# Optimization experiments

Measured on AMD Instinct MI355X. Metric: run time of the kernel, lower is better.

The kernel has to match this reference:

```python
import jax, jax.numpy as jnp
import numpy as np

N = 50000      # nodes
E = 800000     # edges (avg degree 16)
IN = 128       # input feature dim
HID = 32       # per-head hidden dim
H = 4          # attention heads
C = 40         # num classes
SLOPE = 0.2    # leaky relu negative slope


def setup_inputs() -> dict:
    key = jax.random.key(0)
    ks = jax.random.split(key, 14)
    s = 0.05
    inputs = jax.random.normal(ks[0], (N, IN), jnp.float32)
    target = jax.random.normal(ks[1], (N, IN), jnp.float32)
    lamb = jax.random.uniform(ks[2], (1,), jnp.float32)
    src = jax.random.randint(ks[3], (E,), 0, N, jnp.int32)
    dst = jax.random.randint(ks[4], (E,), 0, N, jnp.int32)
    W0 = jax.random.normal(ks[5], (IN, H * HID), jnp.float32) * s
    al0 = jax.random.normal(ks[6], (H, HID), jnp.float32) * s
    ar0 = jax.random.normal(ks[7], (H, HID), jnp.float32) * s
    W1 = jax.random.normal(ks[8], (H * HID, H * HID), jnp.float32) * s
    al1 = jax.random.normal(ks[9], (H, HID), jnp.float32) * s
    ar1 = jax.random.normal(ks[10], (H, HID), jnp.float32) * s
    Wout = jax.random.normal(ks[11], (H * HID, C), jnp.float32) * s
    bout = jnp.zeros((C,), jnp.float32)
    return dict(inputs=inputs, target=target, lamb=lamb,
                W0=W0, al0=al0, ar0=ar0, W1=W1, al1=al1, ar1=ar1,
                Wout=Wout, bout=bout, src=src, dst=dst)


def gat_conv(h, W, al, ar, src, dst, residual):
    # h: [N, in_dim]; W: [in_dim, H*HID]; al/ar: [H, HID]
    feat = (h @ W).reshape(N, H, HID)                  # [N,H,D]
    el = jnp.einsum('nhd,hd->nh', feat, al)            # [N,H]
    er = jnp.einsum('nhd,hd->nh', feat, ar)            # [N,H]
    e = jax.nn.leaky_relu(el[src] + er[dst], SLOPE)    # [E,H]
    # edge softmax over incoming edges of each dst node
    emax = jax.ops.segment_max(e, dst, num_segments=N)  # [N,H]
    ee = jnp.exp(e - emax[dst])                          # [E,H]
    denom = jax.ops.segment_sum(ee, dst, num_segments=N)
    a = ee / denom[dst]                                  # [E,H]
    msg = feat[src] * a[:, :, None]                      # [E,H,D]
    out = jax.ops.segment_sum(msg, dst, num_segments=N)  # [N,H,D]
    if residual:
        out = out + h.reshape(N, H, HID)  # identity residual (in == H*HID)
    return jax.nn.elu(out)


def reference(inputs, target, lamb, W0, al0, ar0, W1, al1, ar1, Wout, bout, src, dst):
    def path(x):
        h = gat_conv(x, W0, al0, ar0, src, dst, residual=False).reshape(N, H * HID)
        h = gat_conv(h, W1, al1, ar1, src, dst, residual=True).reshape(N, H * HID)
        return h

    h = path(inputs)
    h2 = path(target)
    lam = lamb[0]
    h = lam * h + (1.0 - lam) * h2   # mixup_hidden=True
    logits = h @ Wout + bout
    return (h, logits)
```

## Files before the change

kernel.cpp:

```cpp
#include <hip/hip_runtime.h>
#include <hip/hip_bf16.h>
#include <cstddef>

#define GN 50000
#define GE 800000
#define GH 4
#define GD 32
#define SLOPE 0.2f
#define LOG2E 1.4426950408889634f

typedef unsigned short ushort_t;
typedef unsigned int uint_t;
using short8 = __attribute__((ext_vector_type(8))) short;
using float4v = __attribute__((ext_vector_type(4))) float;

__device__ __forceinline__ ushort_t f2bf(float f) {
    union { float f; uint_t u; } v; v.f = f;
    uint_t r = v.u + 0x7fff + ((v.u >> 16) & 1);
    return (ushort_t)(r >> 16);
}
__device__ __forceinline__ float bflo(uint_t u) { return __uint_as_float(u << 16); }
__device__ __forceinline__ float bfhi(uint_t u) { return __uint_as_float(u & 0xffff0000u); }
__device__ __forceinline__ float bfu(ushort_t u) { return __uint_as_float((uint_t)u << 16); }

__device__ __forceinline__ uint_t cvt_pk_bf16(float lo, float hi) {
    uint_t r;
    asm("v_cvt_pk_bf16_f32 %0, %1, %2" : "=v"(r) : "v"(lo), "v"(hi));
    return r;
}

#if __has_builtin(__builtin_amdgcn_exp2f)
#define EXP2F(x) __builtin_amdgcn_exp2f(x)
#else
#define EXP2F(x) exp2f(x)
#endif

#define SWZ_B(v, imm) __uint_as_float((uint_t)__builtin_amdgcn_ds_swizzle((int)__float_as_uint(v), (imm)))

__device__ __forceinline__ int slotmap(int a) {
    return (a < GN) ? (a << 1) : (((a - GN) << 1) | 1);
}

#define NEXT 144
#define WSTRIDE (NEXT * 128)

__global__ void k_hist(const int* __restrict__ dst, int* __restrict__ deg, int E) {
    int i = blockIdx.x * 256 + threadIdx.x;
    if (i < E) atomicAdd(&deg[dst[i]], 1);
}

__global__ void k_scan1(const int* __restrict__ deg, int* __restrict__ row_ptr,
                        int* __restrict__ partials, int n) {
    __shared__ int s[256];
    int t = threadIdx.x;
    int i = blockIdx.x * 256 + t;
    int v = (i < n) ? deg[i] : 0;
    s[t] = v;
    __syncthreads();
    for (int off = 1; off < 256; off <<= 1) {
        int add = (t >= off) ? s[t - off] : 0;
        __syncthreads();
        s[t] += add;
        __syncthreads();
    }
    if (i < n) row_ptr[i] = s[t] - v;
    if (t == 255) partials[blockIdx.x] = s[255];
}

__global__ void k_scan2(int* __restrict__ partials, int nb) {
    __shared__ int s[256];
    int t = threadIdx.x;
    int v = (t < nb) ? partials[t] : 0;
    s[t] = v;
    __syncthreads();
    for (int off = 1; off < 256; off <<= 1) {
        int add = (t >= off) ? s[t - off] : 0;
        __syncthreads();
        s[t] += add;
        __syncthreads();
    }
    if (t < nb) partials[t] = s[t] - v;
}

__global__ void k_scan3(int* __restrict__ row_ptr, int* __restrict__ wpos,
                        const int* __restrict__ partials, int n, int E) {
    int i = blockIdx.x * 256 + threadIdx.x;
    if (i < n) {
        int rp = row_ptr[i] + partials[i >> 8];
        row_ptr[i] = rp;
        wpos[i] = rp;
        if (i == 0) row_ptr[n] = E;
    }
}

__global__ void k_fill(const int* __restrict__ src, const int* __restrict__ dst,
                       int* __restrict__ wpos, int* __restrict__ csr_src, int E) {
    int i = blockIdx.x * 256 + threadIdx.x;
    if (i < E) {
        int p = atomicAdd(&wpos[dst[i]], 1);
        csr_src[p] = src[i];
    }
}

__global__ void k_cvt_all(const float* __restrict__ W0, const float* __restrict__ W1,
                          const float* __restrict__ Wout,
                          const float* __restrict__ al0, const float* __restrict__ ar0,
                          const float* __restrict__ al1, const float* __restrict__ ar1,
                          ushort_t* __restrict__ wbt, ushort_t* __restrict__ woutb) {
    int t = blockIdx.x * 256 + threadIdx.x;
    if (t < 2 * WSTRIDE) {
        int m = t / WSTRIDE;
        int o = t % WSTRIDE;
        int n = o >> 7, k = o & 127;
        const float* W = m ? W1 : W0;
        float v;
        if (n < 128) {
            v = W[k * 128 + n];
        } else if (n < 136) {
            int j = n - 128;
            int h = j & 3;
            const float* a = (j < 4) ? (m ? al1 : al0) : (m ? ar1 : ar0);
            float s = 0.f;
#pragma unroll 8
            for (int d = 0; d < 32; d++) s += W[k * 128 + h * 32 + d] * a[h * 32 + d];
            v = s * LOG2E;
        } else {
            v = 0.f;
        }
        wbt[t] = f2bf(v);
    } else {
        int u = t - 2 * WSTRIDE;
        if (u < 48 * 128) {
            int n = u >> 7, k = u & 127;
            float w = (n < 40) ? Wout[k * 40 + n] : 0.f;
            ushort_t h = f2bf(w);
            woutb[u] = h;
            woutb[48 * 128 + u] = f2bf(w - bfu(h));
        }
    }
}

__device__ __forceinline__ void store_c_ext(ushort_t* __restrict__ Cb,
                                            float* __restrict__ el,
                                            float* __restrict__ er,
                                            const float4v acc[2][9],
                                            int r0, int quad, int col, int M) {
#pragma unroll
    for (int rt = 0; rt < 2; rt++)
#pragma unroll
        for (int nt = 0; nt < 8; nt++) {
            int rb = r0 + rt * 16 + quad * 4;
            int c = nt * 16 + col;
            uint_t p01 = cvt_pk_bf16(acc[rt][nt][0], acc[rt][nt][1]);
            uint_t p23 = cvt_pk_bf16(acc[rt][nt][2], acc[rt][nt][3]);
            if (rb + 0 < M) Cb[(size_t)slotmap(rb + 0) * 128 + c] = (ushort_t)p01;
            if (rb + 1 < M) Cb[(size_t)slotmap(rb + 1) * 128 + c] = (ushort_t)(p01 >> 16);
            if (rb + 2 < M) Cb[(size_t)slotmap(rb + 2) * 128 + c] = (ushort_t)p23;
            if (rb + 3 < M) Cb[(size_t)slotmap(rb + 3) * 128 + c] = (ushort_t)(p23 >> 16);
        }
    if (col < 8) {
        float* dstp = (col < 4) ? el : er;
        int h = col & 3;
#pragma unroll
        for (int rt = 0; rt < 2; rt++)
#pragma unroll
            for (int r = 0; r < 4; r++) {
                int row = r0 + rt * 16 + quad * 4 + r;
                if (row < M) dstp[slotmap(row) * 4 + h] = acc[rt][8][r];
            }
    }
}

__global__ __launch_bounds__(256) void gemm_mfma32(const float* __restrict__ A0,
                                                   const float* __restrict__ A1,
                                                   const ushort_t* __restrict__ WbT,
                                                   ushort_t* __restrict__ Cb,
                                                   float* __restrict__ el,
                                                   float* __restrict__ er, int M) {
    __shared__ ushort_t Bs[NEXT][136];
    int tid = threadIdx.x;
    for (int i = tid; i < NEXT * 16; i += 256) {
        int n = i >> 4;
        int kc = (i & 15) << 3;
        *(short8*)&Bs[n][kc] = *(const short8*)&WbT[n * 128 + kc];
    }
    __syncthreads();
    int wid = tid >> 6, lane = tid & 63;
    int r0 = blockIdx.x * 128 + wid * 32;
    int col = lane & 15, quad = lane >> 4;
    float4v acc[2][9];
#pragma unroll
    for (int rt = 0; rt < 2; rt++)
#pragma unroll
        for (int t = 0; t < 9; t++) acc[rt][t] = (float4v){0.f, 0.f, 0.f, 0.f};
    int ar_[2] = {r0 + col, r0 + 16 + col};
    const float* Ap[2];
#pragma unroll
    for (int rt = 0; rt < 2; rt++) {
        int a = ar_[rt];
        Ap[rt] = (a < M) ? ((a < GN) ? (A0 + (size_t)a * 128)
                                     : (A1 + (size_t)(a - GN) * 128)) : nullptr;
    }
#pragma unroll
    for (int ks = 0; ks < 4; ks++) {
        short8 af[2];
#pragma unroll
        for (int rt = 0; rt < 2; rt++) {
            af[rt] = (short8){};
            if (Ap[rt]) {
                float4 v0 = *(const float4*)&Ap[rt][ks * 32 + quad * 8];
                float4 v1 = *(const float4*)&Ap[rt][ks * 32 + quad * 8 + 4];
                union { short8 s; uint_t u[4]; } cv;
                cv.u[0] = cvt_pk_bf16(v0.x, v0.y);
                cv.u[1] = cvt_pk_bf16(v0.z, v0.w);
                cv.u[2] = cvt_pk_bf16(v1.x, v1.y);
                cv.u[3] = cvt_pk_bf16(v1.z, v1.w);
                af[rt] = cv.s;
            }
        }
#pragma unroll
        for (int nt = 0; nt < 9; nt++) {
            short8 bf = *(const short8*)&Bs[nt * 16 + col][ks * 32 + quad * 8];
            acc[0][nt] = __builtin_amdgcn_mfma_f32_16x16x32_bf16(af[0], bf, acc[0][nt], 0, 0, 0);
            acc[1][nt] = __builtin_amdgcn_mfma_f32_16x16x32_bf16(af[1], bf, acc[1][nt], 0, 0, 0);
        }
    }
    store_c_ext(Cb, el, er, acc, r0, quad, col, M);
}

__global__ __launch_bounds__(256) void gemm_mfma(const ushort_t* __restrict__ A,
                                                 const ushort_t* __restrict__ WbT,
                                                 ushort_t* __restrict__ Cb,
                                                 float* __restrict__ el,
                                                 float* __restrict__ er, int M) {
    __shared__ ushort_t Bs[NEXT][136];
    int tid = threadIdx.x;
    for (int i = tid; i < NEXT * 16; i += 256) {
        int n = i >> 4;
        int kc = (i & 15) << 3;
        *(short8*)&Bs[n][kc] = *(const short8*)&WbT[n * 128 + kc];
    }
    __syncthreads();
    int wid = tid >> 6, lane = tid & 63;
    int r0 = blockIdx.x * 128 + wid * 32;
    int col = lane & 15, quad = lane >> 4;
    float4v acc[2][9];
#pragma unroll
    for (int rt = 0; rt < 2; rt++)
#pragma unroll
        for (int t = 0; t < 9; t++) acc[rt][t] = (float4v){0.f, 0.f, 0.f, 0.f};
    int ar_[2] = {r0 + col, r0 + 16 + col};
    const ushort_t* Ap[2];
#pragma unroll
    for (int rt = 0; rt < 2; rt++) {
        int a = ar_[rt];
        Ap[rt] = (a < M) ? (A + (size_t)slotmap(a) * 128) : nullptr;
    }
#pragma unroll
    for (int ks = 0; ks < 4; ks++) {
        short8 af[2];
#pragma unroll
        for (int rt = 0; rt < 2; rt++) {
            af[rt] = (short8){};
            if (Ap[rt]) af[rt] = *(const short8*)&Ap[rt][ks * 32 + quad * 8];
        }
#pragma unroll
        for (int nt = 0; nt < 9; nt++) {
            short8 bf = *(const short8*)&Bs[nt * 16 + col][ks * 32 + quad * 8];
            acc[0][nt] = __builtin_amdgcn_mfma_f32_16x16x32_bf16(af[0], bf, acc[0][nt], 0, 0, 0);
            acc[1][nt] = __builtin_amdgcn_mfma_f32_16x16x32_bf16(af[1], bf, acc[1][nt], 0, 0, 0);
        }
    }
    store_c_ext(Cb, el, er, acc, r0, quad, col, M);
}

__device__ __forceinline__ void agg_core(
    const ushort_t* __restrict__ featb, const float* __restrict__ el, float ern,
    const int* __restrict__ csr_src, int base, int deg, uint_t eo, uint_t fofs,
    int lk, float& v0, float& v1, float& v2, float& v3) {
    if (deg <= 0) { v0 = v1 = v2 = v3 = 0.f; return; }
    float a0 = 0.f, a1 = 0.f, a2 = 0.f, a3 = 0.f, ss = 0.f;
    int nblk = (deg + 15) >> 4;
    int e1 = base + deg - 1;
    int jb = base;
    int s[16], t[16];
#pragma unroll
    for (int k = 0; k < 16; k++) s[k] = csr_src[min(jb + k, e1)];
    float elA = el[(uint_t)csr_src[min(jb + lk, e1)] * 8u + eo];
    float elB = el[(uint_t)csr_src[min(jb + lk + 8, e1)] * 8u + eo];
    for (int b = 0;;) {
        int rem = deg - (b << 4);
        uint2 f[16];
#pragma unroll
        for (int k = 0; k < 16; k++)
            f[k] = *(const uint2*)&featb[(uint_t)s[k] * 256u + fofs];
        bool more = (b + 1) < nblk;
        float elA2 = 0.f, elB2 = 0.f;
        if (more) {
            int nj = jb + 16;
#pragma unroll
            for (int k = 0; k < 16; k++) t[k] = csr_src[min(nj + k, e1)];
            elA2 = el[(uint_t)csr_src[min(nj + lk, e1)] * 8u + eo];
            elB2 = el[(uint_t)csr_src[min(nj + lk + 8, e1)] * 8u + eo];
        }
        float eA = elA + ern; eA = fmaxf(eA, SLOPE * eA);
        float eB = elB + ern; eB = fmaxf(eB, SLOPE * eB);
        float wA = (lk < rem) ? EXP2F(eA) : 0.f;
        float wB = (lk + 8 < rem) ? EXP2F(eB) : 0.f;
        float wv[16];
        wv[0]  = SWZ_B(wA, 0x018); wv[1]  = SWZ_B(wA, 0x038);
        wv[2]  = SWZ_B(wA, 0x058); wv[3]  = SWZ_B(wA, 0x078);
        wv[4]  = SWZ_B(wA, 0x098); wv[5]  = SWZ_B(wA, 0x0B8);
        wv[6]  = SWZ_B(wA, 0x0D8); wv[7]  = SWZ_B(wA, 0x0F8);
        wv[8]  = SWZ_B(wB, 0x018); wv[9]  = SWZ_B(wB, 0x038);
        wv[10] = SWZ_B(wB, 0x058); wv[11] = SWZ_B(wB, 0x078);
        wv[12] = SWZ_B(wB, 0x098); wv[13] = SWZ_B(wB, 0x0B8);
        wv[14] = SWZ_B(wB, 0x0D8); wv[15] = SWZ_B(wB, 0x0F8);
#pragma unroll
        for (int k = 0; k < 16; k++) {
            float w = wv[k];
            ss += w;
            a0 += w * bflo(f[k].x);
            a1 += w * bfhi(f[k].x);
            a2 += w * bflo(f[k].y);
            a3 += w * bfhi(f[k].y);
        }
        if (!more) break;
        b++; jb += 16;
#pragma unroll
        for (int k = 0; k < 16; k++) s[k] = t[k];
        elA = elA2; elB = elB2;
    }
    float inv = 1.f / ss;
    v0 = a0 * inv; v1 = a1 * inv; v2 = a2 * inv; v3 = a3 * inv;
}

__global__ __launch_bounds__(512) void gat_agg_l1(
    const ushort_t* __restrict__ featb, const float* __restrict__ el,
    const float* __restrict__ er, const int* __restrict__ row_ptr,
    const int* __restrict__ csr_src, ushort_t* __restrict__ abuf) {
    int n = __builtin_amdgcn_readfirstlane(blockIdx.x * 8 + (threadIdx.x >> 6));
    if (n >= GN) return;
    int lane = threadIdx.x & 63;
    int half = lane >> 5;
    int q = lane & 31;
    int lk = lane & 7, q4 = q << 2;
    uint_t eo = (uint_t)(half * 4 + ((lane >> 3) & 3));
    uint_t fofs = (uint_t)(half * 128 + q4);
    float ern = er[(uint_t)n * 8u + eo];
    int base = row_ptr[n];
    int deg = row_ptr[n + 1] - base;
    float v0, v1, v2, v3;
    agg_core(featb, el, ern, csr_src, base, deg, eo, fofs, lk, v0, v1, v2, v3);
    v0 = v0 > 0.f ? v0 : __expf(v0) - 1.f;
    v1 = v1 > 0.f ? v1 : __expf(v1) - 1.f;
    v2 = v2 > 0.f ? v2 : __expf(v2) - 1.f;
    v3 = v3 > 0.f ? v3 : __expf(v3) - 1.f;
    size_t idx = ((size_t)(2 * n + half)) * 128 + q4;
    uint2 o;
    o.x = cvt_pk_bf16(v0, v1);
    o.y = cvt_pk_bf16(v2, v3);
    *(uint2*)&abuf[idx] = o;
}

__global__ __launch_bounds__(512) void gat_agg_l2(
    const ushort_t* __restrict__ featb, const float* __restrict__ el,
    const float* __restrict__ er, const int* __restrict__ row_ptr,
    const int* __restrict__ csr_src, const ushort_t* __restrict__ resid,
    const float* __restrict__ lamb, float* __restrict__ outh) {
    int tid = threadIdx.x;
    int n = __builtin_amdgcn_readfirstlane(blockIdx.x * 8 + (tid >> 6));
    if (n >= GN) return;
    int lane = tid & 63;
    int half = lane >> 5;
    int q = lane & 31;
    int lk = lane & 7, q4 = q << 2;
    uint_t eo = (uint_t)(half * 4 + ((lane >> 3) & 3));
    uint_t fofs = (uint_t)(half * 128 + q4);
    float ern = er[(uint_t)n * 8u + eo];
    int base = row_ptr[n];
    int deg = row_ptr[n + 1] - base;
    float v0, v1, v2, v3;
    agg_core(featb, el, ern, csr_src, base, deg, eo, fofs, lk, v0, v1, v2, v3);
    size_t idx = ((size_t)(2 * n + half)) * 128 + q4;
    ushort4 r = *(const ushort4*)&resid[idx];
    v0 += bfu(r.x); v1 += bfu(r.y); v2 += bfu(r.z); v3 += bfu(r.w);
    v0 = v0 > 0.f ? v0 : __expf(v0) - 1.f;
    v1 = v1 > 0.f ? v1 : __expf(v1) - 1.f;
    v2 = v2 > 0.f ? v2 : __expf(v2) - 1.f;
    v3 = v3 > 0.f ? v3 : __expf(v3) - 1.f;
    float p0 = __shfl_xor(v0, 32, 64);
    float p1 = __shfl_xor(v1, 32, 64);
    float p2 = __shfl_xor(v2, 32, 64);
    float p3 = __shfl_xor(v3, 32, 64);
    float lam = lamb[0];
    if (half == 0) {
        float m0 = lam * v0 + (1.f - lam) * p0;
        float m1 = lam * v1 + (1.f - lam) * p1;
        float m2 = lam * v2 + (1.f - lam) * p2;
        float m3 = lam * v3 + (1.f - lam) * p3;
        *(float4*)&outh[(size_t)n * 128 + q4] = make_float4(m0, m1, m2, m3);
    }
}

__global__ __launch_bounds__(256) void k_logits(const float* __restrict__ Hf,
                                                const ushort_t* __restrict__ Wb,
                                                const float* __restrict__ bout,
                                                float* __restrict__ outlog) {
    __shared__ ushort_t Bh[48][136];
    __shared__ ushort_t Bl[48][136];
    int tid = threadIdx.x;
    for (int i = tid; i < 48 * 16; i += 256) {
        int n = i >> 4;
        int kc = (i & 15) << 3;
        *(short8*)&Bh[n][kc] = *(const short8*)&Wb[n * 128 + kc];
        *(short8*)&Bl[n][kc] = *(const short8*)&Wb[48 * 128 + n * 128 + kc];
    }
    __syncthreads();
    int wid = tid >> 6, lane = tid & 63;
    int r0 = blockIdx.x * 128 + wid * 32;
    int col = lane & 15, quad = lane >> 4;
    float4v acc[2][3];
#pragma unroll
    for (int rt = 0; rt < 2; rt++)
#pragma unroll
        for (int nt = 0; nt < 3; nt++) acc[rt][nt] = (float4v){0.f, 0.f, 0.f, 0.f};
    int ar_[2] = {r0 + col, r0 + 16 + col};
#pragma unroll
    for (int ks = 0; ks < 4; ks++) {
        short8 ah[2], alo[2];
#pragma unroll
        for (int rt = 0; rt < 2; rt++) {
            ah[rt] = (short8){};
            alo[rt] = (short8){};
            if (ar_[rt] < GN) {
                const float* p = Hf + (size_t)ar_[rt] * 128 + ks * 32 + quad * 8;
                float4 x = *(const float4*)p;
                float4 y = *(const float4*)(p + 4);
                union { short8 s; uint_t u[4]; } ch, cl;
                ch.u[0] = cvt_pk_bf16(x.x, x.y);
                ch.u[1] = cvt_pk_bf16(x.z, x.w);
                ch.u[2] = cvt_pk_bf16(y.x, y.y);
                ch.u[3] = cvt_pk_bf16(y.z, y.w);
                cl.u[0] = cvt_pk_bf16(x.x - bflo(ch.u[0]), x.y - bfhi(ch.u[0]));
                cl.u[1] = cvt_pk_bf16(x.z - bflo(ch.u[1]), x.w - bfhi(ch.u[1]));
                cl.u[2] = cvt_pk_bf16(y.x - bflo(ch.u[2]), y.y - bfhi(ch.u[2]));
                cl.u[3] = cvt_pk_bf16(y.z - bflo(ch.u[3]), y.w - bfhi(ch.u[3]));
                ah[rt] = ch.s;
                alo[rt] = cl.s;
            }
        }
#pragma unroll
        for (int nt = 0; nt < 3; nt++) {
            short8 bh = *(const short8*)&Bh[nt * 16 + col][ks * 32 + quad * 8];
            short8 bl = *(const short8*)&Bl[nt * 16 + col][ks * 32 + quad * 8];
#pragma unroll
            for (int rt = 0; rt < 2; rt++) {
                acc[rt][nt] = __builtin_amdgcn_mfma_f32_16x16x32_bf16(ah[rt], bh, acc[rt][nt], 0, 0, 0);
                acc[rt][nt] = __builtin_amdgcn_mfma_f32_16x16x32_bf16(alo[rt], bh, acc[rt][nt], 0, 0, 0);
                acc[rt][nt] = __builtin_amdgcn_mfma_f32_16x16x32_bf16(ah[rt], bl, acc[rt][nt], 0, 0, 0);
            }
        }
    }
#pragma unroll
    for (int nt = 0; nt < 3; nt++) {
        int c = nt * 16 + col;
        if (c < 40) {
            float bv = bout[c];
#pragma unroll
            for (int rt = 0; rt < 2; rt++)
#pragma unroll
                for (int r = 0; r < 4; r++) {
                    int row = r0 + rt * 16 + quad * 4 + r;
                    if (row < GN) outlog[(size_t)row * 40 + c] = acc[rt][nt][r] + bv;
                }
        }
    }
}

extern "C" void kernel_launch(void* const* d_in, const int* in_sizes, int n_in,
                              void* d_out, int out_size, void* d_ws, size_t ws_size,
                              hipStream_t stream) {
    const float* inputs = (const float*)d_in[0];
    const float* target = (const float*)d_in[1];
    const float* lamb   = (const float*)d_in[2];
    const float* W0     = (const float*)d_in[3];
    const float* al0    = (const float*)d_in[4];
    const float* ar0    = (const float*)d_in[5];
    const float* W1     = (const float*)d_in[6];
    const float* al1    = (const float*)d_in[7];
    const float* ar1    = (const float*)d_in[8];
    const float* Wout   = (const float*)d_in[9];
    const float* bout   = (const float*)d_in[10];
    const int*   src    = (const int*)d_in[11];
    const int*   dst    = (const int*)d_in[12];

    float* out = (float*)d_out;
    float* outh = out;
    float* outlog = out + (size_t)GN * 128;

    const int NP = 2 * GN;
    ushort_t* featb = (ushort_t*)d_ws;
    ushort_t* abuf  = featb + (size_t)NP * 128;
    float* el = (float*)(abuf + (size_t)NP * 128);
    float* er = el + (size_t)NP * GH;
    ushort_t* wbt = (ushort_t*)(er + (size_t)NP * GH);
    int* row_ptr  = (int*)(wbt + 2 * WSTRIDE);
    int* wpos     = row_ptr + (GN + 1);
    int* csr_src  = wpos + GN;
    int* partials = csr_src + GE + 16;
    ushort_t* woutb = (ushort_t*)(partials + 256);

    const int nb = (GN + 255) / 256;
    const int eb = (GE + 255) / 256;
    const int gblocks = (NP + 127) / 128;
    const int aggblocks = (GN + 7) / 8;
    const int lblocks = (GN + 127) / 128;
    const int cvtblocks = (2 * WSTRIDE + 48 * 128 + 255) / 256;

    hipMemsetAsync(wpos, 0, GN * sizeof(int), stream);
    k_hist<<<eb, 256, 0, stream>>>(dst, wpos, GE);
    k_scan1<<<nb, 256, 0, stream>>>(wpos, row_ptr, partials, GN);
    k_scan2<<<1, 256, 0, stream>>>(partials, nb);
    k_scan3<<<nb, 256, 0, stream>>>(row_ptr, wpos, partials, GN, GE);
    k_fill<<<eb, 256, 0, stream>>>(src, dst, wpos, csr_src, GE);

    k_cvt_all<<<cvtblocks, 256, 0, stream>>>(W0, W1, Wout, al0, ar0, al1, ar1,
                                             wbt, woutb);

    gemm_mfma32<<<gblocks, 256, 0, stream>>>(inputs, target, wbt,
                                             featb, el, er, NP);
    gat_agg_l1<<<aggblocks, 512, 0, stream>>>(featb, el, er, row_ptr, csr_src, abuf);

    gemm_mfma<<<gblocks, 256, 0, stream>>>(abuf, wbt + WSTRIDE,
                                           featb, el, er, NP);
    gat_agg_l2<<<aggblocks, 512, 0, stream>>>(featb, el, er, row_ptr, csr_src,
                                              abuf, lamb, outh);

    k_logits<<<lblocks, 256, 0, stream>>>(outh, woutb, bout, outlog);
}
```

Before: 382.2 us.

## Fuse weight conversion with degree histogram and record edge ranks to drop fill atomics

Weight conversion and the in-degree histogram now run as one launch, with extra blocks doing the histogram. Each edge's atomicAdd return value is kept as its rank within its destination, so the CSR fill becomes plain indexed stores (row_ptr + rank) with no second round of atomics. Both edge kernels process four edges per thread using int4 loads. The cost is an extra E-sized rank array written and read back. Edge order inside each CSR row is still set by atomic arrival order, as before.

```diff
diff --git a/kernel.cpp b/kernel.cpp
--- a/kernel.cpp
+++ b/kernel.cpp
@@ -44,69 +44,27 @@
 #define NEXT 144
 #define WSTRIDE (NEXT * 128)
 
-__global__ void k_hist(const int* __restrict__ dst, int* __restrict__ deg, int E) {
-    int i = blockIdx.x * 256 + threadIdx.x;
-    if (i < E) atomicAdd(&deg[dst[i]], 1);
-}
-
-__global__ void k_scan1(const int* __restrict__ deg, int* __restrict__ row_ptr,
-                        int* __restrict__ partials, int n) {
-    __shared__ int s[256];
-    int t = threadIdx.x;
-    int i = blockIdx.x * 256 + t;
-    int v = (i < n) ? deg[i] : 0;
-    s[t] = v;
-    __syncthreads();
-    for (int off = 1; off < 256; off <<= 1) {
-        int add = (t >= off) ? s[t - off] : 0;
-        __syncthreads();
-        s[t] += add;
-        __syncthreads();
-    }
-    if (i < n) row_ptr[i] = s[t] - v;
-    if (t == 255) partials[blockIdx.x] = s[255];
-}
-
-__global__ void k_scan2(int* __restrict__ partials, int nb) {
-    __shared__ int s[256];
-    int t = threadIdx.x;
-    int v = (t < nb) ? partials[t] : 0;
-    s[t] = v;
-    __syncthreads();
-    for (int off = 1; off < 256; off <<= 1) {
-        int add = (t >= off) ? s[t - off] : 0;
-        __syncthreads();
-        s[t] += add;
-        __syncthreads();
-    }
-    if (t < nb) partials[t] = s[t] - v;
-}
-
-__global__ void k_scan3(int* __restrict__ row_ptr, int* __restrict__ wpos,
-                        const int* __restrict__ partials, int n, int E) {
-    int i = blockIdx.x * 256 + threadIdx.x;
-    if (i < n) {
-        int rp = row_ptr[i] + partials[i >> 8];
-        row_ptr[i] = rp;
-        wpos[i] = rp;
-        if (i == 0) row_ptr[n] = E;
-    }
-}
-
-__global__ void k_fill(const int* __restrict__ src, const int* __restrict__ dst,
-                       int* __restrict__ wpos, int* __restrict__ csr_src, int E) {
-    int i = blockIdx.x * 256 + threadIdx.x;
-    if (i < E) {
-        int p = atomicAdd(&wpos[dst[i]], 1);
-        csr_src[p] = src[i];
-    }
-}
-
-__global__ void k_cvt_all(const float* __restrict__ W0, const float* __restrict__ W1,
-                          const float* __restrict__ Wout,
-                          const float* __restrict__ al0, const float* __restrict__ ar0,
-                          const float* __restrict__ al1, const float* __restrict__ ar1,
-                          ushort_t* __restrict__ wbt, ushort_t* __restrict__ woutb) {
+__global__ __launch_bounds__(256) void k_cvt_hist(
+    const float* __restrict__ W0, const float* __restrict__ W1,
+    const float* __restrict__ Wout,
+    const float* __restrict__ al0, const float* __restrict__ ar0,
+    const float* __restrict__ al1, const float* __restrict__ ar1,
+    ushort_t* __restrict__ wbt, ushort_t* __restrict__ woutb,
+    const int* __restrict__ dst, int* __restrict__ deg, int* __restrict__ rank,
+    int cvtb, int E) {
+    if ((int)blockIdx.x >= cvtb) {
+        int i = ((blockIdx.x - cvtb) * 256 + threadIdx.x) * 4;
+        if (i + 3 < E) {
+            int4 d = *(const int4*)&dst[i];
+            rank[i + 0] = atomicAdd(&deg[d.x], 1);
+            rank[i + 1] = atomicAdd(&deg[d.y], 1);
+            rank[i + 2] = atomicAdd(&deg[d.z], 1);
+            rank[i + 3] = atomicAdd(&deg[d.w], 1);
+        } else {
+            for (int k = i; k < E; k++) rank[k] = atomicAdd(&deg[dst[k]], 1);
+        }
+        return;
+    }
     int t = blockIdx.x * 256 + threadIdx.x;
     if (t < 2 * WSTRIDE) {
         int m = t / WSTRIDE;
@@ -137,6 +95,66 @@
             woutb[u] = h;
             woutb[48 * 128 + u] = f2bf(w - bfu(h));
         }
+    }
+}
+
+__global__ void k_scan1(const int* __restrict__ deg, int* __restrict__ row_ptr,
+                        int* __restrict__ partials, int n) {
+    __shared__ int s[256];
+    int t = threadIdx.x;
+    int i = blockIdx.x * 256 + t;
+    int v = (i < n) ? deg[i] : 0;
+    s[t] = v;
+    __syncthreads();
+    for (int off = 1; off < 256; off <<= 1) {
+        int add = (t >= off) ? s[t - off] : 0;
+        __syncthreads();
+        s[t] += add;
+        __syncthreads();
+    }
+    if (i < n) row_ptr[i] = s[t] - v;
+    if (t == 255) partials[blockIdx.x] = s[255];
+}
+
+__global__ void k_scan2(int* __restrict__ partials, int nb) {
+    __shared__ int s[256];
+    int t = threadIdx.x;
+    int v = (t < nb) ? partials[t] : 0;
+    s[t] = v;
+    __syncthreads();
+    for (int off = 1; off < 256; off <<= 1) {
+        int add = (t >= off) ? s[t - off] : 0;
+        __syncthreads();
+        s[t] += add;
+        __syncthreads();
+    }
+    if (t < nb) partials[t] = s[t] - v;
+}
+
+__global__ void k_scan3(int* __restrict__ row_ptr,
+                        const int* __restrict__ partials, int n, int E) {
+    int i = blockIdx.x * 256 + threadIdx.x;
+    if (i < n) {
+        row_ptr[i] += partials[i >> 8];
+        if (i == 0) row_ptr[n] = E;
+    }
+}
+
+__global__ void k_fill(const int* __restrict__ src, const int* __restrict__ dst,
+                       const int* __restrict__ rank, const int* __restrict__ row_ptr,
+                       int* __restrict__ csr_src, int E) {
+    int i = (blockIdx.x * 256 + threadIdx.x) * 4;
+    if (i + 3 < E) {
+        int4 d = *(const int4*)&dst[i];
+        int4 s = *(const int4*)&src[i];
+        int4 r = *(const int4*)&rank[i];
+        csr_src[row_ptr[d.x] + r.x] = s.x;
+        csr_src[row_ptr[d.y] + r.y] = s.y;
+        csr_src[row_ptr[d.z] + r.z] = s.z;
+        csr_src[row_ptr[d.w] + r.w] = s.w;
+    } else {
+        for (int k = i; k < E; k++)
+            csr_src[row_ptr[dst[k]] + rank[k]] = src[k];
     }
 }
 
@@ -509,24 +527,26 @@
     int* wpos     = row_ptr + (GN + 1);
     int* csr_src  = wpos + GN;
     int* partials = csr_src + GE + 16;
-    ushort_t* woutb = (ushort_t*)(partials + 256);
+    int* rank     = partials + 256;
+    ushort_t* woutb = (ushort_t*)(rank + GE + 16);
 
     const int nb = (GN + 255) / 256;
-    const int eb = (GE + 255) / 256;
+    const int eb4 = (GE / 4 + 255) / 256;
     const int gblocks = (NP + 127) / 128;
     const int aggblocks = (GN + 7) / 8;
     const int lblocks = (GN + 127) / 128;
     const int cvtblocks = (2 * WSTRIDE + 48 * 128 + 255) / 256;
 
     hipMemsetAsync(wpos, 0, GN * sizeof(int), stream);
-    k_hist<<<eb, 256, 0, stream>>>(dst, wpos, GE);
+    k_cvt_hist<<<cvtblocks + eb4, 256, 0, stream>>>(W0, W1, Wout, al0, ar0, al1, ar1,
+                                                    wbt, woutb, dst, wpos, rank,
+                                                    cvtblocks, GE);
+
     k_scan1<<<nb, 256, 0, stream>>>(wpos, row_ptr, partials, GN);
     k_scan2<<<1, 256, 0, stream>>>(partials, nb);
-    k_scan3<<<nb, 256, 0, stream>>>(row_ptr, wpos, partials, GN, GE);
-    k_fill<<<eb, 256, 0, stream>>>(src, dst, wpos, csr_src, GE);
-
-    k_cvt_all<<<cvtblocks, 256, 0, stream>>>(W0, W1, Wout, al0, ar0, al1, ar1,
-                                             wbt, woutb);
+    k_scan3<<<nb, 256, 0, stream>>>(row_ptr, partials, GN, GE);
+
+    k_fill<<<eb4, 256, 0, stream>>>(src, dst, rank, row_ptr, csr_src, GE);
 
     gemm_mfma32<<<gblocks, 256, 0, stream>>>(inputs, target, wbt,
                                              featb, el, er, NP);
```

Result: faster. 348.8 us (-8.7%).
